# Kernel optimization log

Hardware: AMD Instinct MI355X
Metric: run time of the kernel (lower is better)

## Reference

```python
import jax, jax.numpy as jnp
import numpy as np

D_MODEL = 1024
NUM_HEADS = 16
NUM_GROUPS = 4
HEAD_DIM = D_MODEL // NUM_HEADS
ROPE_BASE = 10000.0


def _rope_tables(seq_len, head_dim, dtype=jnp.float32):
    inv_freq = 1.0 / (ROPE_BASE ** (jnp.arange(0, head_dim, 2, dtype=jnp.float32) / head_dim))
    freqs = jnp.arange(seq_len, dtype=jnp.float32)[:, None] * inv_freq[None, :]  # [S, hd/2]
    emb = jnp.concatenate([freqs, freqs], axis=-1)  # [S, hd]
    return jnp.cos(emb).astype(dtype), jnp.sin(emb).astype(dtype)


def _rotate_half(t):
    half = t.shape[-1] // 2
    return jnp.concatenate([-t[..., half:], t[..., :half]], axis=-1)


def _apply_rope(t, cos, sin):
    # t: [B,S,H,hd]; cos/sin: [S,hd] broadcast over batch and heads
    c = cos[None, :, None, :]
    s = sin[None, :, None, :]
    return t * c + _rotate_half(t) * s


def setup_inputs() -> dict:
    key = jax.random.key(0)
    ks = jax.random.split(key, 5)
    B, S, D = 2, 2048, D_MODEL
    scale = 1.0 / np.sqrt(D)
    return {
        "x": jax.random.normal(ks[0], (B, S, D), dtype=jnp.float32),
        "Wq": jax.random.normal(ks[1], (D, D), dtype=jnp.float32) * scale,
        "Wk": jax.random.normal(ks[2], (D, D), dtype=jnp.float32) * scale,
        "Wv": jax.random.normal(ks[3], (D, D), dtype=jnp.float32) * scale,
        "Wo": jax.random.normal(ks[4], (D, D), dtype=jnp.float32) * scale,
    }


def reference(x, Wq, Wk, Wv, Wo):
    B, S, D = x.shape
    H, G, hd = NUM_HEADS, NUM_GROUPS, HEAD_DIM
    hpg = H // G  # heads per group

    q = (x @ Wq.T).reshape(B, S, H, hd)
    k = (x @ Wk.T).reshape(B, S, H, hd)
    v = (x @ Wv.T).reshape(B, S, H, hd)

    cos, sin = _rope_tables(S, hd, x.dtype)
    q = _apply_rope(q, cos, sin)
    k = _apply_rope(k, cos, sin)

    # query head reordering: [B,S,G,hpg,hd] -> transpose(2,3) -> [B,S,H,hd]
    q = q.reshape(B, S, G, hpg, hd).swapaxes(2, 3).reshape(B, S, H, hd)
    # GQA group-mean of K/V, then repeat back to H heads
    k = k.reshape(B, S, G, hpg, hd).mean(axis=3)  # [B,S,G,hd]
    v = v.reshape(B, S, G, hpg, hd).mean(axis=3)
    k = jnp.repeat(k, hpg, axis=2)  # [B,S,H,hd]
    v = jnp.repeat(v, hpg, axis=2)

    q = q.transpose(0, 2, 1, 3)  # [B,H,S,hd]
    k = k.transpose(0, 2, 1, 3)
    v = v.transpose(0, 2, 1, 3)

    scores = jnp.einsum('bhqd,bhkd->bhqk', q, k) / np.sqrt(hd)  # [B,H,S,S]
    probs = jax.nn.softmax(scores, axis=-1)
    attn = jnp.einsum('bhqk,bhkd->bhqd', probs, v)

    attn = attn.transpose(0, 2, 1, 3).reshape(B, S, D)
    return attn @ Wo.T
```

## Files before the change

kernel.cpp:

```cpp
#include <hip/hip_runtime.h>
#include <hip/hip_bf16.h>
#include <math.h>

#define B_ 2
#define S_ 2048
#define D_ 1024
#define H_ 16
#define G_ 4
#define HD_ 64

typedef float f32x4  __attribute__((ext_vector_type(4)));
typedef float f32x16 __attribute__((ext_vector_type(16)));
typedef short s16x8  __attribute__((ext_vector_type(8)));
typedef unsigned short u16x4 __attribute__((ext_vector_type(4)));
typedef unsigned int   u32x4 __attribute__((ext_vector_type(4)));

__device__ __forceinline__ unsigned short f2b(float f) {
    __hip_bfloat16 h = __float2bfloat16(f);
    return __builtin_bit_cast(unsigned short, h);
}
__device__ __forceinline__ float b2f(unsigned short u) {
    return __builtin_bit_cast(float, (unsigned)u << 16);
}
__device__ __forceinline__ unsigned cvtpk(float lo, float hi) {
    unsigned r;
    asm("v_cvt_pk_bf16_f32 %0, %1, %2" : "=v"(r) : "v"(lo), "v"(hi));
    return r;
}
__device__ __forceinline__ void plswap(unsigned &a, unsigned &b) {
    asm("v_permlane32_swap_b32 %0, %1" : "+v"(a), "+v"(b));
}

#define MFMA16(a, b, c) __builtin_amdgcn_mfma_f32_16x16x32_bf16(a, b, c, 0, 0, 0)
#define MFMA32(a, b, c) __builtin_amdgcn_mfma_f32_32x32x16_bf16(a, b, c, 0, 0, 0)

#define GLOAD16(gp, lp) __builtin_amdgcn_global_load_lds(                      \
    (const __attribute__((address_space(1))) void*)(gp),                      \
    (__attribute__((address_space(3))) void*)(lp), 16, 0, 0)

__global__ __launch_bounds__(256)
void prep_all(const float* __restrict__ x,  const float* __restrict__ Wq,
              const float* __restrict__ Wk, const float* __restrict__ Wv,
              const float* __restrict__ Wo,
              unsigned short* __restrict__ xb, unsigned short* __restrict__ wb,
              unsigned short* __restrict__ wob,
              float* __restrict__ cost, float* __restrict__ sint)
{
    const int NQ_WB = (1536*1024)/4;
    const int NQ_WO = (1024*1024)/4;
    const int NQ_X  = (B_*S_*D_)/4;
    int q = blockIdx.x*256 + threadIdx.x;
    if (q < NQ_WB) {
        const int idx = q*4, row = idx >> 10, c = idx & 1023;
        u16x4 o;
        if (row < 1024) {
            f32x4 v = *(const f32x4*)&Wq[(size_t)row*1024 + c];
            #pragma unroll
            for (int j = 0; j < 4; ++j) o[j] = f2b(v[j]);
        } else {
            const int rd = row - 1024, kv = rd >> 8, gd = rd & 255;
            const int g = gd >> 6, d = gd & 63;
            const float* W = kv ? Wv : Wk;
            f32x4 sum = {0.f, 0.f, 0.f, 0.f};
            #pragma unroll
            for (int p = 0; p < 4; ++p)
                sum += *(const f32x4*)&W[(size_t)((g*4 + p)*64 + d)*1024 + c];
            #pragma unroll
            for (int j = 0; j < 4; ++j) o[j] = f2b(sum[j]*0.25f);
        }
        *(u16x4*)&wb[idx] = o;
        return;
    }
    q -= NQ_WB;
    if (q < NQ_WO) {
        const int idx = q*4;
        f32x4 v = *(const f32x4*)&Wo[idx];
        u16x4 o;
        #pragma unroll
        for (int j = 0; j < 4; ++j) o[j] = f2b(v[j]);
        *(u16x4*)&wob[idx] = o;
        return;
    }
    q -= NQ_WO;
    if (q < NQ_X) {
        const int idx = q*4;
        f32x4 v = *(const f32x4*)&x[idx];
        u16x4 o;
        #pragma unroll
        for (int j = 0; j < 4; ++j) o[j] = f2b(v[j]);
        *(u16x4*)&xb[idx] = o;
        return;
    }
    q -= NQ_X;
    if (q < (S_*32)/4) {
        const int idx = q*4, s = idx >> 5, f0 = idx & 31;
        #pragma unroll
        for (int j = 0; j < 4; ++j) {
            const float f = (float)(f0 + j);
            const float fr = (float)s * powf(10000.0f, -f*(1.0f/32.0f));
            cost[idx + j] = cosf(fr);
            sint[idx + j] = sinf(fr);
        }
    }
}

template<int MODE>
__global__ __launch_bounds__(256)
void gemm_mfma(const unsigned short* __restrict__ Am,
               const unsigned short* __restrict__ Bm,
               unsigned short* __restrict__ qr,
               unsigned short* __restrict__ kr,
               unsigned short* __restrict__ vt,
               float* __restrict__ outf,
               const float* __restrict__ cost,
               const float* __restrict__ sint,
               int nbx)
{
    __shared__ unsigned short As[2][128*64];
    __shared__ unsigned short Bs[2][128*64];

    const int nwg = gridDim.x;
    const int cpx = nwg >> 3;
    const int bid = blockIdx.x;
    const int swz = (bid & 7)*cpx + (bid >> 3);
    const int bx = swz % nbx, by = swz / nbx;

    const int t  = threadIdx.x;
    const int w  = t >> 6, l = t & 63;
    const int lg = l >> 4, lr = l & 15;
    const int wr = w >> 1, wc = w & 1;

    const unsigned short* gA = Am + (size_t)by*128*D_;
    const unsigned short* gB = Bm + (size_t)bx*128*D_;

    const int srow = l >> 3;
    const int schk = (l & 7) ^ srow;

#define STAGE(buf, k0)                                                         \
    _Pragma("unroll")                                                          \
    for (int i_ = 0; i_ < 4; ++i_) {                                           \
        const int row_ = 32*w + 8*i_ + srow;                                   \
        GLOAD16(gA + (size_t)row_*D_ + (k0) + 8*schk, &As[buf][(32*w + 8*i_)*64]); \
        GLOAD16(gB + (size_t)row_*D_ + (k0) + 8*schk, &Bs[buf][(32*w + 8*i_)*64]); \
    }

    f32x4 acc[4][4] = {};

    STAGE(0, 0);
    #pragma unroll 1
    for (int kt = 0; kt < 16; ++kt) {
        const int cur = kt & 1;
        if (kt < 15) {
            STAGE(cur ^ 1, 64*(kt + 1));
            asm volatile("s_waitcnt vmcnt(8)" ::: "memory");
        } else {
            asm volatile("s_waitcnt vmcnt(0)" ::: "memory");
        }
        __builtin_amdgcn_s_barrier();

        #pragma unroll
        for (int kk = 0; kk < 2; ++kk) {
            s16x8 af[4], bfr[4];
            #pragma unroll
            for (int m = 0; m < 4; ++m) {
                const int row = 64*wr + 16*m + lr;
                af[m] = *(const s16x8*)&As[cur][row*64 + 8*((lg + 4*kk) ^ (row & 7))];
            }
            #pragma unroll
            for (int n = 0; n < 4; ++n) {
                const int col = 64*wc + 16*n + lr;
                bfr[n] = *(const s16x8*)&Bs[cur][col*64 + 8*((lg + 4*kk) ^ (col & 7))];
            }
            #pragma unroll
            for (int m = 0; m < 4; ++m)
                #pragma unroll
                for (int n = 0; n < 4; ++n)
                    acc[m][n] = MFMA16(af[m], bfr[n], acc[m][n]);
        }
        asm volatile("s_waitcnt lgkmcnt(0)" ::: "memory");
        __builtin_amdgcn_s_barrier();
    }
#undef STAGE

    if (MODE == 1) {
        #pragma unroll
        for (int m = 0; m < 4; ++m)
            #pragma unroll
            for (int r = 0; r < 4; ++r) {
                const int row = by*128 + 64*wr + 16*m + 4*lg + r;
                #pragma unroll
                for (int n = 0; n < 4; ++n)
                    outf[(size_t)row*D_ + bx*128 + 64*wc + 16*n + lr] = acc[m][n][r];
            }
        return;
    }

    if (bx < 10) {
        const float CQ = 0.18033688011112044f;
        #pragma unroll
        for (int m = 0; m < 4; ++m) {
            #pragma unroll
            for (int r = 0; r < 4; ++r) {
                const int row = by*128 + 64*wr + 16*m + 4*lg + r;
                const int b = row >> 11, s = row & (S_ - 1);
                const float c_lo = cost[s*32 + lr],      s_lo = sint[s*32 + lr];
                const float c_hi = cost[s*32 + 16 + lr], s_hi = sint[s*32 + 16 + lr];
                unsigned short vals[4];
                #pragma unroll
                for (int n = 0; n < 4; ++n) {
                    const float cc = (n & 1) ? c_hi : c_lo;
                    const float sn = (n & 1) ? s_hi : s_lo;
                    const float self = acc[m][n][r], part = acc[m][n ^ 2][r];
                    float rv = (n < 2) ? fmaf(self, cc, -part*sn)
                                       : fmaf(self, cc,  part*sn);
                    if (bx < 8) rv *= CQ;
                    vals[n] = f2b(rv);
                }
                size_t base;
                unsigned short* dst;
                if (bx < 8) {
                    const int hh = 2*bx + wc;
                    const int hp = (hh & 3)*4 + (hh >> 2);
                    base = (((size_t)b*H_ + hp)*S_ + s)*HD_;
                    dst = qr;
                } else {
                    const int g = (bx - 8)*2 + wc;
                    base = (((size_t)b*G_ + g)*S_ + s)*HD_;
                    dst = kr;
                }
                #pragma unroll
                for (int n = 0; n < 4; ++n) dst[base + 16*n + lr] = vals[n];
            }
        }
    } else {
        const int g = (bx - 10)*2 + wc;
        #pragma unroll
        for (int m = 0; m < 4; ++m) {
            const int row0 = by*128 + 64*wr + 16*m + 4*lg;
            const int b = row0 >> 11, s0 = row0 & (S_ - 1);
            #pragma unroll
            for (int n = 0; n < 4; ++n) {
                const int dd = 16*n + lr;
                u16x4 v;
                #pragma unroll
                for (int r = 0; r < 4; ++r) v[r] = f2b(acc[m][n][r]);
                *(u16x4*)&vt[(((size_t)b*G_ + g)*HD_ + dd)*S_ + s0] = v;
            }
        }
    }
}

__device__ __forceinline__ void stage64(const unsigned short* Kp, const unsigned short* Vp,
                                        unsigned short* ks, unsigned short* vs,
                                        int key0, int w, int l)
{
    const int srow = l >> 3;
    const int schk = (l & 7) ^ srow;
    #pragma unroll
    for (int i = 0; i < 2; ++i) {
        const int row = 16*w + 8*i + srow;
        GLOAD16(Kp + ((size_t)(key0 + row))*HD_ + 8*schk, ks + (16*w + 8*i)*64);
        GLOAD16(Vp + (size_t)row*S_ + key0 + 8*schk,      vs + (16*w + 8*i)*64);
    }
}

__global__ __launch_bounds__(256, 4)
void flash_attn_mfma(const unsigned short* __restrict__ qr,
                     const unsigned short* __restrict__ kr,
                     const unsigned short* __restrict__ vt,
                     unsigned short* __restrict__ po,
                     float* __restrict__ pl)
{
    __shared__ unsigned short Ks[2][64*64];
    __shared__ unsigned short Vs[2][64*64];

    const int bid  = blockIdx.x;
    const int cpx  = gridDim.x >> 3;
    const int swz  = (bid & 7)*cpx + (bid >> 3);
    const int qt   = swz & 15;
    const int h    = (swz >> 4) & 15;
    const int b    = (swz >> 8) & 1;
    const int half = swz >> 9;
    const int g    = h >> 2;
    const int t    = threadIdx.x;
    const int w    = t >> 6;
    const int l    = t & 63;
    const int hi   = l >> 5;
    const int li   = l & 31;

    const unsigned short* Qp = qr + (((size_t)b*H_ + h)*S_ + (size_t)qt*128 + w*32)*HD_;
    const unsigned short* Kp = kr + ((size_t)b*G_ + g)*(size_t)S_*HD_ + (size_t)half*1024*HD_;
    const unsigned short* Vp = vt + ((size_t)b*G_ + g)*(size_t)HD_*S_ + half*1024;

    s16x8 qf[4];
    #pragma unroll
    for (int kk = 0; kk < 4; ++kk)
        qf[kk] = *(const s16x8*)(Qp + (size_t)li*HD_ + 16*kk + 8*hi);

    s16x8 ones;
    #pragma unroll
    for (int e = 0; e < 8; ++e) ones[e] = (short)0x3F80;

    f32x16 o[2], o_l;
    #pragma unroll
    for (int e = 0; e < 16; ++e) { o[0][e] = 0.f; o[1][e] = 0.f; o_l[e] = 0.f; }

    const int NT = 1024/64;
    stage64(Kp, Vp, Ks[0], Vs[0], 0, w, l);

    #pragma unroll 1
    for (int kt = 0; kt < NT; ++kt) {
        const int cur = kt & 1;
        if (kt + 1 < NT) {
            stage64(Kp, Vp, Ks[cur^1], Vs[cur^1], 64*(kt + 1), w, l);
            asm volatile("s_waitcnt vmcnt(4)" ::: "memory");
        } else {
            asm volatile("s_waitcnt vmcnt(0)" ::: "memory");
        }
        __builtin_amdgcn_s_barrier();

        f32x16 sc[2];
        #pragma unroll
        for (int q4 = 0; q4 < 2; ++q4)
            #pragma unroll
            for (int e = 0; e < 16; ++e) sc[q4][e] = 0.f;

        __builtin_amdgcn_s_setprio(1);
        #pragma unroll
        for (int kk = 0; kk < 4; ++kk) {
            const int chk = 8*((hi + 2*kk) ^ (li & 7));
            #pragma unroll
            for (int q4 = 0; q4 < 2; ++q4) {
                s16x8 kf = *(const s16x8*)&Ks[cur][(32*q4 + li)*64 + chk];
                sc[q4] = MFMA32(kf, qf[kk], sc[q4]);
            }
        }
        __builtin_amdgcn_s_setprio(0);

        #pragma unroll
        for (int q4 = 0; q4 < 2; ++q4)
            #pragma unroll
            for (int e = 0; e < 16; ++e)
                sc[q4][e] = __builtin_amdgcn_exp2f(sc[q4][e]);

        __builtin_amdgcn_s_setprio(1);
        #pragma unroll
        for (int q4 = 0; q4 < 2; ++q4) {
            #pragma unroll
            for (int s2 = 0; s2 < 2; ++s2) {
                unsigned a0 = cvtpk(sc[q4][8*s2+0], sc[q4][8*s2+1]);
                unsigned a1 = cvtpk(sc[q4][8*s2+2], sc[q4][8*s2+3]);
                unsigned a2 = cvtpk(sc[q4][8*s2+4], sc[q4][8*s2+5]);
                unsigned a3 = cvtpk(sc[q4][8*s2+6], sc[q4][8*s2+7]);
                plswap(a0, a2); plswap(a1, a3);
                u32x4 aw = {a0, a1, a2, a3};
                s16x8 paf = __builtin_bit_cast(s16x8, aw);
                const int ks = 2*q4 + s2;
                #pragma unroll
                for (int dt = 0; dt < 2; ++dt) {
                    const int d = li + 32*dt;
                    s16x8 vf = *(const s16x8*)&Vs[cur][d*64 + 8*((hi + 2*ks) ^ (li & 7))];
                    o[dt] = MFMA32(paf, vf, o[dt]);
                }
                o_l = MFMA32(paf, ones, o_l);
            }
        }
        __builtin_amdgcn_s_setprio(0);

        asm volatile("s_waitcnt lgkmcnt(0)" ::: "memory");
        __builtin_amdgcn_s_barrier();
    }

    const size_t pbase = (((size_t)half*B_ + b)*H_ + h)*S_;
    #pragma unroll
    for (int r = 0; r < 16; ++r) {
        const int qq = (r & 3) + 8*(r >> 2) + 4*hi;
        const int s  = qt*128 + w*32 + qq;
        #pragma unroll
        for (int dt = 0; dt < 2; ++dt)
            po[(pbase + s)*HD_ + li + 32*dt] = f2b(o[dt][r]);
        if (li == 0) pl[pbase + s] = o_l[r];
    }
}

__global__ __launch_bounds__(256)
void combine_kernel(const unsigned short* __restrict__ po,
                    const float* __restrict__ pl,
                    unsigned short* __restrict__ attnb)
{
    const int i  = blockIdx.x*256 + threadIdx.x;
    const int d8 = i & 7;
    const int s  = (i >> 3) & (S_ - 1);
    const int h  = (i >> 14) & (H_ - 1);
    const int b  = i >> 18;
    const size_t r0 = (((size_t)b)*H_ + h)*S_ + s;
    const size_t r1 = (((size_t)B_ + b)*H_ + h)*S_ + s;
    const float inv = 1.0f / (pl[r0] + pl[r1]);
    s16x8 p0 = *(const s16x8*)&po[r0*HD_ + d8*8];
    s16x8 p1 = *(const s16x8*)&po[r1*HD_ + d8*8];
    s16x8 ov;
    #pragma unroll
    for (int j = 0; j < 8; ++j) {
        const float v = (b2f((unsigned short)p0[j]) + b2f((unsigned short)p1[j])) * inv;
        ov[j] = (short)f2b(v);
    }
    *(s16x8*)&attnb[((size_t)b*S_ + s)*D_ + h*HD_ + d8*8] = ov;
}

extern "C" void kernel_launch(void* const* d_in, const int* in_sizes, int n_in,
                              void* d_out, int out_size, void* d_ws, size_t ws_size,
                              hipStream_t stream)
{
    const float* x  = (const float*)d_in[0];
    const float* Wq = (const float*)d_in[1];
    const float* Wk = (const float*)d_in[2];
    const float* Wv = (const float*)d_in[3];
    const float* Wo = (const float*)d_in[4];
    float* out = (float*)d_out;

    char* p = (char*)d_ws;
    unsigned short* qr    = (unsigned short*)p; p += (size_t)B_*H_*S_*HD_*2;
    unsigned short* kr    = (unsigned short*)p; p += (size_t)B_*G_*S_*HD_*2;
    unsigned short* vt    = (unsigned short*)p; p += (size_t)B_*G_*HD_*S_*2;
    unsigned short* wob   = (unsigned short*)p; p += (size_t)1024*1024*2;
    unsigned short* attnb = (unsigned short*)p; p += (size_t)B_*S_*D_*2;
    float* pl   = (float*)p;  p += (size_t)2*B_*H_*S_*4;
    float* cost = (float*)p;  p += (size_t)S_*32*4;
    float* sint = (float*)p;  p += (size_t)S_*32*4;
    char* regionX = p;
    unsigned short* xb = (unsigned short*)regionX;
    unsigned short* wb = (unsigned short*)(regionX + (size_t)B_*S_*D_*2);
    unsigned short* po = (unsigned short*)regionX;

    prep_all<<<6720, 256, 0, stream>>>(x, Wq, Wk, Wv, Wo, xb, wb, wob, cost, sint);
    gemm_mfma<0><<<32*12, 256, 0, stream>>>(xb, wb, qr, kr, vt, nullptr, cost, sint, 12);
    flash_attn_mfma<<<B_*H_*(S_/128)*2, 256, 0, stream>>>(qr, kr, vt, po, pl);
    combine_kernel<<<(B_*H_*S_*HD_/8)/256, 256, 0, stream>>>(po, pl, attnb);
    gemm_mfma<1><<<32*8, 256, 0, stream>>>(attnb, wob, nullptr, nullptr, nullptr, out, cost, sint, 8);
}
```

Before: 105.6 us.

## Fuse split-KV combine into attention block and halve GEMM M-tile

The attention kernel now launches 512-thread blocks in which two halves of the waves each process half the keys. The two partial results are merged through shared memory and written straight to the bf16 attention buffer, which removes the separate combine kernel and the partial-output round trip through global memory. Separately, the GEMM tile shrinks from 128x128 to 64x128, doubling the grid to improve CU occupancy and wave balance on the small projections. The cost is less reuse per tile in the GEMMs, a doubled LDS footprint plus extra barriers in attention, and a workspace layout that no longer aliases buffers.

```diff
diff --git a/kernel.cpp b/kernel.cpp
--- a/kernel.cpp
+++ b/kernel.cpp
@@ -18,9 +18,6 @@
 __device__ __forceinline__ unsigned short f2b(float f) {
     __hip_bfloat16 h = __float2bfloat16(f);
     return __builtin_bit_cast(unsigned short, h);
-}
-__device__ __forceinline__ float b2f(unsigned short u) {
-    return __builtin_bit_cast(float, (unsigned)u << 16);
 }
 __device__ __forceinline__ unsigned cvtpk(float lo, float hi) {
     unsigned r;
@@ -116,7 +113,7 @@
                const float* __restrict__ sint,
                int nbx)
 {
-    __shared__ unsigned short As[2][128*64];
+    __shared__ unsigned short As[2][64*64];
     __shared__ unsigned short Bs[2][128*64];
 
     const int nwg = gridDim.x;
@@ -130,7 +127,7 @@
     const int lg = l >> 4, lr = l & 15;
     const int wr = w >> 1, wc = w & 1;
 
-    const unsigned short* gA = Am + (size_t)by*128*D_;
+    const unsigned short* gA = Am + (size_t)by*64*D_;
     const unsigned short* gB = Bm + (size_t)bx*128*D_;
 
     const int srow = l >> 3;
@@ -138,13 +135,17 @@
 
 #define STAGE(buf, k0)                                                         \
     _Pragma("unroll")                                                          \
+    for (int i_ = 0; i_ < 2; ++i_) {                                           \
+        const int rowA_ = 16*w + 8*i_ + srow;                                  \
+        GLOAD16(gA + (size_t)rowA_*D_ + (k0) + 8*schk, &As[buf][(16*w + 8*i_)*64]); \
+    }                                                                          \
+    _Pragma("unroll")                                                          \
     for (int i_ = 0; i_ < 4; ++i_) {                                           \
-        const int row_ = 32*w + 8*i_ + srow;                                   \
-        GLOAD16(gA + (size_t)row_*D_ + (k0) + 8*schk, &As[buf][(32*w + 8*i_)*64]); \
-        GLOAD16(gB + (size_t)row_*D_ + (k0) + 8*schk, &Bs[buf][(32*w + 8*i_)*64]); \
-    }
-
-    f32x4 acc[4][4] = {};
+        const int rowB_ = 32*w + 8*i_ + srow;                                  \
+        GLOAD16(gB + (size_t)rowB_*D_ + (k0) + 8*schk, &Bs[buf][(32*w + 8*i_)*64]); \
+    }
+
+    f32x4 acc[2][4] = {};
 
     STAGE(0, 0);
     #pragma unroll 1
@@ -152,7 +153,7 @@
         const int cur = kt & 1;
         if (kt < 15) {
             STAGE(cur ^ 1, 64*(kt + 1));
-            asm volatile("s_waitcnt vmcnt(8)" ::: "memory");
+            asm volatile("s_waitcnt vmcnt(6)" ::: "memory");
         } else {
             asm volatile("s_waitcnt vmcnt(0)" ::: "memory");
         }
@@ -160,10 +161,10 @@
 
         #pragma unroll
         for (int kk = 0; kk < 2; ++kk) {
-            s16x8 af[4], bfr[4];
-            #pragma unroll
-            for (int m = 0; m < 4; ++m) {
-                const int row = 64*wr + 16*m + lr;
+            s16x8 af[2], bfr[4];
+            #pragma unroll
+            for (int m = 0; m < 2; ++m) {
+                const int row = 32*wr + 16*m + lr;
                 af[m] = *(const s16x8*)&As[cur][row*64 + 8*((lg + 4*kk) ^ (row & 7))];
             }
             #pragma unroll
@@ -172,7 +173,7 @@
                 bfr[n] = *(const s16x8*)&Bs[cur][col*64 + 8*((lg + 4*kk) ^ (col & 7))];
             }
             #pragma unroll
-            for (int m = 0; m < 4; ++m)
+            for (int m = 0; m < 2; ++m)
                 #pragma unroll
                 for (int n = 0; n < 4; ++n)
                     acc[m][n] = MFMA16(af[m], bfr[n], acc[m][n]);
@@ -184,10 +185,10 @@
 
     if (MODE == 1) {
         #pragma unroll
-        for (int m = 0; m < 4; ++m)
+        for (int m = 0; m < 2; ++m)
             #pragma unroll
             for (int r = 0; r < 4; ++r) {
-                const int row = by*128 + 64*wr + 16*m + 4*lg + r;
+                const int row = by*64 + 32*wr + 16*m + 4*lg + r;
                 #pragma unroll
                 for (int n = 0; n < 4; ++n)
                     outf[(size_t)row*D_ + bx*128 + 64*wc + 16*n + lr] = acc[m][n][r];
@@ -198,10 +199,10 @@
     if (bx < 10) {
         const float CQ = 0.18033688011112044f;
         #pragma unroll
-        for (int m = 0; m < 4; ++m) {
+        for (int m = 0; m < 2; ++m) {
             #pragma unroll
             for (int r = 0; r < 4; ++r) {
-                const int row = by*128 + 64*wr + 16*m + 4*lg + r;
+                const int row = by*64 + 32*wr + 16*m + 4*lg + r;
                 const int b = row >> 11, s = row & (S_ - 1);
                 const float c_lo = cost[s*32 + lr],      s_lo = sint[s*32 + lr];
                 const float c_hi = cost[s*32 + 16 + lr], s_hi = sint[s*32 + 16 + lr];
@@ -235,8 +236,8 @@
     } else {
         const int g = (bx - 10)*2 + wc;
         #pragma unroll
-        for (int m = 0; m < 4; ++m) {
-            const int row0 = by*128 + 64*wr + 16*m + 4*lg;
+        for (int m = 0; m < 2; ++m) {
+            const int row0 = by*64 + 32*wr + 16*m + 4*lg;
             const int b = row0 >> 11, s0 = row0 & (S_ - 1);
             #pragma unroll
             for (int n = 0; n < 4; ++n) {
@@ -264,26 +265,26 @@
     }
 }
 
-__global__ __launch_bounds__(256, 4)
+__global__ __launch_bounds__(512, 4)
 void flash_attn_mfma(const unsigned short* __restrict__ qr,
                      const unsigned short* __restrict__ kr,
                      const unsigned short* __restrict__ vt,
-                     unsigned short* __restrict__ po,
-                     float* __restrict__ pl)
+                     unsigned short* __restrict__ attnb)
 {
-    __shared__ unsigned short Ks[2][64*64];
-    __shared__ unsigned short Vs[2][64*64];
+    __shared__ unsigned short Ks[2][2][64*64];
+    __shared__ unsigned short Vs[2][2][64*64];
 
     const int bid  = blockIdx.x;
     const int cpx  = gridDim.x >> 3;
     const int swz  = (bid & 7)*cpx + (bid >> 3);
     const int qt   = swz & 15;
     const int h    = (swz >> 4) & 15;
-    const int b    = (swz >> 8) & 1;
-    const int half = swz >> 9;
+    const int b    = swz >> 8;
     const int g    = h >> 2;
     const int t    = threadIdx.x;
-    const int w    = t >> 6;
+    const int w8   = t >> 6;
+    const int half = w8 >> 2;
+    const int w    = w8 & 3;
     const int l    = t & 63;
     const int hi   = l >> 5;
     const int li   = l & 31;
@@ -306,13 +307,13 @@
     for (int e = 0; e < 16; ++e) { o[0][e] = 0.f; o[1][e] = 0.f; o_l[e] = 0.f; }
 
     const int NT = 1024/64;
-    stage64(Kp, Vp, Ks[0], Vs[0], 0, w, l);
+    stage64(Kp, Vp, Ks[half][0], Vs[half][0], 0, w, l);
 
     #pragma unroll 1
     for (int kt = 0; kt < NT; ++kt) {
         const int cur = kt & 1;
         if (kt + 1 < NT) {
-            stage64(Kp, Vp, Ks[cur^1], Vs[cur^1], 64*(kt + 1), w, l);
+            stage64(Kp, Vp, Ks[half][cur^1], Vs[half][cur^1], 64*(kt + 1), w, l);
             asm volatile("s_waitcnt vmcnt(4)" ::: "memory");
         } else {
             asm volatile("s_waitcnt vmcnt(0)" ::: "memory");
@@ -331,7 +332,7 @@
             const int chk = 8*((hi + 2*kk) ^ (li & 7));
             #pragma unroll
             for (int q4 = 0; q4 < 2; ++q4) {
-                s16x8 kf = *(const s16x8*)&Ks[cur][(32*q4 + li)*64 + chk];
+                s16x8 kf = *(const s16x8*)&Ks[half][cur][(32*q4 + li)*64 + chk];
                 sc[q4] = MFMA32(kf, qf[kk], sc[q4]);
             }
         }
@@ -359,7 +360,7 @@
                 #pragma unroll
                 for (int dt = 0; dt < 2; ++dt) {
                     const int d = li + 32*dt;
-                    s16x8 vf = *(const s16x8*)&Vs[cur][d*64 + 8*((hi + 2*ks) ^ (li & 7))];
+                    s16x8 vf = *(const s16x8*)&Vs[half][cur][d*64 + 8*((hi + 2*ks) ^ (li & 7))];
                     o[dt] = MFMA32(paf, vf, o[dt]);
                 }
                 o_l = MFMA32(paf, ones, o_l);
@@ -371,40 +372,34 @@
         __builtin_amdgcn_s_barrier();
     }
 
-    const size_t pbase = (((size_t)half*B_ + b)*H_ + h)*S_;
-    #pragma unroll
-    for (int r = 0; r < 16; ++r) {
-        const int qq = (r & 3) + 8*(r >> 2) + 4*hi;
-        const int s  = qt*128 + w*32 + qq;
-        #pragma unroll
-        for (int dt = 0; dt < 2; ++dt)
-            po[(pbase + s)*HD_ + li + 32*dt] = f2b(o[dt][r]);
-        if (li == 0) pl[pbase + s] = o_l[r];
-    }
-}
-
-__global__ __launch_bounds__(256)
-void combine_kernel(const unsigned short* __restrict__ po,
-                    const float* __restrict__ pl,
-                    unsigned short* __restrict__ attnb)
-{
-    const int i  = blockIdx.x*256 + threadIdx.x;
-    const int d8 = i & 7;
-    const int s  = (i >> 3) & (S_ - 1);
-    const int h  = (i >> 14) & (H_ - 1);
-    const int b  = i >> 18;
-    const size_t r0 = (((size_t)b)*H_ + h)*S_ + s;
-    const size_t r1 = (((size_t)B_ + b)*H_ + h)*S_ + s;
-    const float inv = 1.0f / (pl[r0] + pl[r1]);
-    s16x8 p0 = *(const s16x8*)&po[r0*HD_ + d8*8];
-    s16x8 p1 = *(const s16x8*)&po[r1*HD_ + d8*8];
-    s16x8 ov;
-    #pragma unroll
-    for (int j = 0; j < 8; ++j) {
-        const float v = (b2f((unsigned short)p0[j]) + b2f((unsigned short)p1[j])) * inv;
-        ov[j] = (short)f2b(v);
-    }
-    *(s16x8*)&attnb[((size_t)b*S_ + s)*D_ + h*HD_ + d8*8] = ov;
+    float* ocomb = (float*)&Ks[0][0][0];
+    float* lcomb = (float*)&Vs[0][0][0];
+    __syncthreads();
+
+    if (half == 1) {
+        #pragma unroll
+        for (int r = 0; r < 16; ++r) {
+            const int qq  = (r & 3) + 8*(r >> 2) + 4*hi;
+            const int row = w*32 + qq;
+            ocomb[row*64 + li]      = o[0][r];
+            ocomb[row*64 + li + 32] = o[1][r];
+            if (li == 0) lcomb[row] = o_l[r];
+        }
+    }
+    __syncthreads();
+    if (half == 0) {
+        #pragma unroll
+        for (int r = 0; r < 16; ++r) {
+            const int qq  = (r & 3) + 8*(r >> 2) + 4*hi;
+            const int row = w*32 + qq;
+            const int s   = qt*128 + row;
+            const float inv = 1.0f / (o_l[r] + lcomb[row]);
+            const float v0 = (o[0][r] + ocomb[row*64 + li])      * inv;
+            const float v1 = (o[1][r] + ocomb[row*64 + li + 32]) * inv;
+            attnb[((size_t)b*S_ + s)*D_ + h*HD_ + li]      = f2b(v0);
+            attnb[((size_t)b*S_ + s)*D_ + h*HD_ + li + 32] = f2b(v1);
+        }
+    }
 }
 
 extern "C" void kernel_launch(void* const* d_in, const int* in_sizes, int n_in,
@@ -419,22 +414,18 @@
     float* out = (float*)d_out;
 
     char* p = (char*)d_ws;
+    unsigned short* xb    = (unsigned short*)p; p += (size_t)B_*S_*D_*2;
+    unsigned short* wb    = (unsigned short*)p; p += (size_t)1536*1024*2;
+    unsigned short* wob   = (unsigned short*)p; p += (size_t)1024*1024*2;
     unsigned short* qr    = (unsigned short*)p; p += (size_t)B_*H_*S_*HD_*2;
     unsigned short* kr    = (unsigned short*)p; p += (size_t)B_*G_*S_*HD_*2;
     unsigned short* vt    = (unsigned short*)p; p += (size_t)B_*G_*HD_*S_*2;
-    unsigned short* wob   = (unsigned short*)p; p += (size_t)1024*1024*2;
     unsigned short* attnb = (unsigned short*)p; p += (size_t)B_*S_*D_*2;
-    float* pl   = (float*)p;  p += (size_t)2*B_*H_*S_*4;
-    float* cost = (float*)p;  p += (size_t)S_*32*4;
-    float* sint = (float*)p;  p += (size_t)S_*32*4;
-    char* regionX = p;
-    unsigned short* xb = (unsigned short*)regionX;
-    unsigned short* wb = (unsigned short*)(regionX + (size_t)B_*S_*D_*2);
-    unsigned short* po = (unsigned short*)regionX;
+    float* cost = (float*)p; p += (size_t)S_*32*4;
+    float* sint = (float*)p;
 
     prep_all<<<6720, 256, 0, stream>>>(x, Wq, Wk, Wv, Wo, xb, wb, wob, cost, sint);
-    gemm_mfma<0><<<32*12, 256, 0, stream>>>(xb, wb, qr, kr, vt, nullptr, cost, sint, 12);
-    flash_attn_mfma<<<B_*H_*(S_/128)*2, 256, 0, stream>>>(qr, kr, vt, po, pl);
-    combine_kernel<<<(B_*H_*S_*HD_/8)/256, 256, 0, stream>>>(po, pl, attnb);
-    gemm_mfma<1><<<32*8, 256, 0, stream>>>(attnb, wob, nullptr, nullptr, nullptr, out, cost, sint, 8);
-}
+    gemm_mfma<0><<<64*12, 256, 0, stream>>>(xb, wb, qr, kr, vt, nullptr, cost, sint, 12);
+    flash_attn_mfma<<<B_*H_*(S_/128), 512, 0, stream>>>(qr, kr, vt, attnb);
+    gemm_mfma<1><<<64*8, 256, 0, stream>>>(attnb, wob, nullptr, nullptr, nullptr, out, cost, sint, 8);
+}
```

Result: faster. 99.13 us (-6.2%).
